# Kernel tuning notes

Hardware: AMD Instinct MI355X
Metric: run time of the kernel (lower is better)

## Reference

```python
import jax, jax.numpy as jnp
import numpy as np
import math

N, D_IN, D_OUT = 65536, 512, 512

def setup_inputs() -> dict:
    key = jax.random.key(0)
    k1, k2 = jax.random.split(key)
    x = jax.random.normal(k1, (N, D_IN), dtype=jnp.float32)
    stdv = 1.0 / math.sqrt(D_OUT)
    W = jax.random.uniform(k2, (D_OUT, D_IN), dtype=jnp.float32, minval=-stdv, maxval=stdv)
    W = W.at[:, 0].set(0.0)  # reset_parameters zeroes column 0 (step == in_features)
    b = jnp.zeros((D_OUT,), dtype=jnp.float32)
    scale = jnp.asarray(math.log(10.0), dtype=jnp.float32)  # learned log-scale param
    return {"x": x, "W": W, "b": b, "scale": scale}

def reference(x, W, b, scale):
    # Linear (dropout is identity at inference; nonlin is None)
    y = jnp.einsum('ni,oi->no', x, W) + b               # [N, D_OUT]
    time = jax.nn.sigmoid(y[..., :1]) * jnp.exp(scale) + 1.1   # [N, 1]
    x_narrow = y[..., 1:]                               # [N, D_OUT-1]
    denom = jnp.clip(jnp.sum(x_narrow * x_narrow, axis=-1, keepdims=True), 1e-8, None)
    s = (time * time - 1.0) / denom                     # [N, 1]
    return jnp.concatenate([time, x_narrow * jnp.sqrt(s)], axis=-1)
```

## Files before the change

### kernel.cpp

```cpp
#include <hip/hip_runtime.h>
#include <stdint.h>


typedef short short8 __attribute__((ext_vector_type(8)));
typedef unsigned short ushort4v __attribute__((ext_vector_type(4)));
typedef float f32x4 __attribute__((ext_vector_type(4)));

#define THREADS 512
#define BM 64
#define KTILES 16
#define LDS_W(buf) ((buf) * 32768)
#define LDS_X(buf) (65536 + (buf) * 4096)

__device__ __forceinline__ unsigned short f2bf(float f) {
  union { float f; uint32_t u; } v; v.f = f;
  uint32_t u = v.u;
  return (unsigned short)((u + 0x7FFFu + ((u >> 16) & 1u)) >> 16);
}

__device__ __forceinline__ void gload_lds16(const void* g, void* l) {
  __builtin_amdgcn_global_load_lds(
      (const __attribute__((address_space(1))) void*)g,
      (__attribute__((address_space(3))) void*)l, 16, 0, 0);
}

__global__ void wconv_kernel(const float* __restrict__ w,
                             unsigned short* __restrict__ wb) {
  const int i = (blockIdx.x * blockDim.x + threadIdx.x) * 4;
  float4 f = *(const float4*)(w + i);
  ushort4v h;
  h[0] = f2bf(f.x); h[1] = f2bf(f.y); h[2] = f2bf(f.z); h[3] = f2bf(f.w);
  *(ushort4v*)(wb + i) = h;
}

__global__ __launch_bounds__(THREADS, 4) void lorentz_kernel(
    const float* __restrict__ xg, const unsigned short* __restrict__ wb,
    const float* __restrict__ bg, const float* __restrict__ sg,
    float* __restrict__ out) {
  __shared__ __align__(16) char smem[73728];
  const int t = threadIdx.x;
  const int lane = t & 63;
  const int wid = t >> 6;
  const int wm = wid >> 2;
  const int wn = wid & 3;
  const int l15 = lane & 15;
  const int q = lane >> 4;
  const int bm = blockIdx.x * BM;
  const int swzl = ((l15 >> 1) & 3) << 4;

  const int wrow0 = t >> 2;
  const int wslog = (t & 3) ^ ((wrow0 >> 1) & 3);
  const unsigned short* wsrc0 = wb + wrow0 * 512 + wslog * 8;
  const int xm = t >> 3;
  const int xk4 = (t & 7) << 2;
  const float* xsrc0 = xg + (bm + xm) * 512 + xk4;
  const int xdst_off = xm * 64 + ((xk4 << 1) ^ ((((xm) >> 1) & 3) << 4));

  f32x4 acc[2][8];
  #pragma unroll
  for (int a = 0; a < 2; ++a)
    #pragma unroll
    for (int n = 0; n < 8; ++n)
      acc[a][n] = (f32x4){0.f, 0.f, 0.f, 0.f};

  auto stage = [&](int buf, int kt) {
    const float* xs = xsrc0 + kt * 32;
    float4 f0 = *(const float4*)xs;
    const unsigned short* ws = wsrc0 + kt * 32;
    char* wd = smem + LDS_W(buf) + t * 16;
    #pragma unroll
    for (int i = 0; i < 4; ++i)
      gload_lds16(ws + i * 65536, wd + i * 8192);
    ushort4v h;
    h[0] = f2bf(f0.x); h[1] = f2bf(f0.y); h[2] = f2bf(f0.z); h[3] = f2bf(f0.w);
    *(ushort4v*)(smem + LDS_X(buf) + xdst_off) = h;
  };

  auto compute = [&](int buf) {
    const char* wsrc = smem + LDS_W(buf);
    const char* xsrc = smem + LDS_X(buf);
    const int kb = q * 16;
    short8 af[2];
    #pragma unroll
    for (int mr = 0; mr < 2; ++mr) {
      const int row = wm * 32 + mr * 16 + l15;
      af[mr] = *(const short8*)(xsrc + row * 64 + (kb ^ swzl));
    }
    #pragma unroll
    for (int nr = 0; nr < 8; ++nr) {
      const int row = wn * 128 + nr * 16 + l15;
      const short8 bf = *(const short8*)(wsrc + row * 64 + (kb ^ swzl));
      acc[0][nr] = __builtin_amdgcn_mfma_f32_16x16x32_bf16(af[0], bf,
                                                           acc[0][nr], 0, 0, 0);
      acc[1][nr] = __builtin_amdgcn_mfma_f32_16x16x32_bf16(af[1], bf,
                                                           acc[1][nr], 0, 0, 0);
    }
  };

  stage(0, 0);
  __syncthreads();
  #pragma unroll
  for (int kt = 0; kt < KTILES; ++kt) {
    const int cur = kt & 1;
    if (kt + 1 < KTILES) stage(cur ^ 1, kt + 1);
    compute(cur);
    __syncthreads();
  }

  const float esc = __expf(sg[0]);
  float* red = (float*)smem;
  float* tsh = red + 64;
  if (t < 64) red[t] = 0.f;

  float bv[8];
  #pragma unroll
  for (int nr = 0; nr < 8; ++nr) bv[nr] = bg[wn * 128 + nr * 16 + l15];
  #pragma unroll
  for (int mr = 0; mr < 2; ++mr)
    #pragma unroll
    for (int nr = 0; nr < 8; ++nr)
      #pragma unroll
      for (int j = 0; j < 4; ++j)
        acc[mr][nr][j] += bv[nr];

  const bool col0 = (wn == 0) && (l15 == 0);
  float ps[2][4];
  #pragma unroll
  for (int mr = 0; mr < 2; ++mr)
    #pragma unroll
    for (int j = 0; j < 4; ++j) {
      float s = 0.f;
      #pragma unroll
      for (int nr = 0; nr < 8; ++nr) { const float v = acc[mr][nr][j]; s += v * v; }
      if (col0) { const float v = acc[mr][0][j]; s -= v * v; }
      ps[mr][j] = s;
    }
  #pragma unroll
  for (int msk = 1; msk < 16; msk <<= 1)
    #pragma unroll
    for (int mr = 0; mr < 2; ++mr)
      #pragma unroll
      for (int j = 0; j < 4; ++j)
        ps[mr][j] += __shfl_xor(ps[mr][j], msk, 64);

  __syncthreads();
  if (l15 == 0) {
    #pragma unroll
    for (int mr = 0; mr < 2; ++mr)
      #pragma unroll
      for (int j = 0; j < 4; ++j)
        atomicAdd(&red[wm * 32 + mr * 16 + q * 4 + j], ps[mr][j]);
  }
  if (col0) {
    #pragma unroll
    for (int mr = 0; mr < 2; ++mr)
      #pragma unroll
      for (int j = 0; j < 4; ++j) {
        const float y0 = acc[mr][0][j];
        const float sgm = 1.f / (1.f + __expf(-y0));
        tsh[wm * 32 + mr * 16 + q * 4 + j] = sgm * esc + 1.1f;
      }
  }
  __syncthreads();

  #pragma unroll
  for (int mr = 0; mr < 2; ++mr)
    #pragma unroll
    for (int j = 0; j < 4; ++j) {
      const int r = wm * 32 + mr * 16 + q * 4 + j;
      float denom = red[r];
      denom = denom < 1e-8f ? 1e-8f : denom;
      const float tt = tsh[r];
      const float coef = sqrtf((tt * tt - 1.f) / denom);
      float* orow = out + (size_t)(bm + r) * 512;
      #pragma unroll
      for (int nr = 0; nr < 8; ++nr) {
        const int c = wn * 128 + nr * 16 + l15;
        orow[c] = (c == 0) ? tt : acc[mr][nr][j] * coef;
      }
    }
}

extern "C" void kernel_launch(void* const* d_in, const int* in_sizes, int n_in,
                              void* d_out, int out_size, void* d_ws, size_t ws_size,
                              hipStream_t stream) {
  const float* x = (const float*)d_in[0];
  const float* W = (const float*)d_in[1];
  const float* b = (const float*)d_in[2];
  const float* sc = (const float*)d_in[3];
  float* outp = (float*)d_out;
  unsigned short* wb = (unsigned short*)d_ws;

  wconv_kernel<<<256, 256, 0, stream>>>(W, wb);
  lorentz_kernel<<<65536 / BM, THREADS, 0, stream>>>(x, wb, b, sc, outp);
}
```

Before: 259.4 us.

## Switch to 32x32x16 MFMA with triple-buffered K=16 pipeline and prefetch distance two

Replaces the 16x16x32 MFMA tiling with 32x32x16 bf16 MFMAs (four accumulators per wave) and shrinks the K tile to 16. Staging is now triple-buffered with a prefetch distance of two, uses explicit waitcnt and barrier, and raises MFMA priority with setprio. The aim is to cut LDS traffic per FLOP, lower LDS footprint for better occupancy, and overlap global loads with compute. The cost is twice as many barriers per K, and the unswizzled LDS layout may cause bank conflicts.

```diff
diff --git a/kernel.cpp b/kernel.cpp
--- a/kernel.cpp
+++ b/kernel.cpp
@@ -3,14 +3,14 @@
 
 
 typedef short short8 __attribute__((ext_vector_type(8)));
+typedef float f32x16 __attribute__((ext_vector_type(16)));
 typedef unsigned short ushort4v __attribute__((ext_vector_type(4)));
-typedef float f32x4 __attribute__((ext_vector_type(4)));
 
 #define THREADS 512
 #define BM 64
-#define KTILES 16
-#define LDS_W(buf) ((buf) * 32768)
-#define LDS_X(buf) (65536 + (buf) * 4096)
+#define WTILE 16384
+#define XTILE 2048
+#define PHASE (WTILE + XTILE)
 
 __device__ __forceinline__ unsigned short f2bf(float f) {
   union { float f; uint32_t u; } v; v.f = f;
@@ -37,148 +37,151 @@
     const float* __restrict__ xg, const unsigned short* __restrict__ wb,
     const float* __restrict__ bg, const float* __restrict__ sg,
     float* __restrict__ out) {
-  __shared__ __align__(16) char smem[73728];
+  __shared__ __align__(16) char smem[3 * PHASE];
   const int t = threadIdx.x;
   const int lane = t & 63;
   const int wid = t >> 6;
   const int wm = wid >> 2;
   const int wn = wid & 3;
-  const int l15 = lane & 15;
-  const int q = lane >> 4;
+  const int l31 = lane & 31;
+  const int h = lane >> 5;
   const int bm = blockIdx.x * BM;
-  const int swzl = ((l15 >> 1) & 3) << 4;
 
-  const int wrow0 = t >> 2;
-  const int wslog = (t & 3) ^ ((wrow0 >> 1) & 3);
-  const unsigned short* wsrc0 = wb + wrow0 * 512 + wslog * 8;
-  const int xm = t >> 3;
-  const int xk4 = (t & 7) << 2;
-  const float* xsrc0 = xg + (bm + xm) * 512 + xk4;
-  const int xdst_off = xm * 64 + ((xk4 << 1) ^ ((((xm) >> 1) & 3) << 4));
+  char* const P0 = smem;
+  char* const P1 = smem + PHASE;
+  char* const P2 = smem + 2 * PHASE;
 
-  f32x4 acc[2][8];
+  const unsigned short* wsrc0 = wb + (t >> 1) * 512 + (t & 1) * 8;
+  const float* xsrc0 = xg + (size_t)(bm + (t >> 3)) * 512 + (t & 7) * 2;
+  const int wdst = t * 16;
+  const int xdst = WTILE + (t >> 3) * 32 + (t & 7) * 4;
+  const int aoff = WTILE + wm * 1024 + l31 * 32 + h * 16;
+  const int boff = (wn * 128 + l31) * 32 + h * 16;
+
+  f32x16 acc[4];
   #pragma unroll
-  for (int a = 0; a < 2; ++a)
+  for (int n = 0; n < 4; ++n)
     #pragma unroll
-    for (int n = 0; n < 8; ++n)
-      acc[a][n] = (f32x4){0.f, 0.f, 0.f, 0.f};
+    for (int j = 0; j < 16; ++j) acc[n][j] = 0.f;
 
-  auto stage = [&](int buf, int kt) {
-    const float* xs = xsrc0 + kt * 32;
-    float4 f0 = *(const float4*)xs;
-    const unsigned short* ws = wsrc0 + kt * 32;
-    char* wd = smem + LDS_W(buf) + t * 16;
-    #pragma unroll
-    for (int i = 0; i < 4; ++i)
-      gload_lds16(ws + i * 65536, wd + i * 8192);
-    ushort4v h;
-    h[0] = f2bf(f0.x); h[1] = f2bf(f0.y); h[2] = f2bf(f0.z); h[3] = f2bf(f0.w);
-    *(ushort4v*)(smem + LDS_X(buf) + xdst_off) = h;
+  {
+    float2 xv0 = *(const float2*)(xsrc0);
+    gload_lds16(wsrc0, P0 + wdst);
+    gload_lds16(wsrc0 + 131072, P0 + 8192 + wdst);
+    unsigned int p0 = (unsigned int)f2bf(xv0.x) | ((unsigned int)f2bf(xv0.y) << 16);
+    *(unsigned int*)(P0 + xdst) = p0;
+    float2 xv1 = *(const float2*)(xsrc0 + 16);
+    gload_lds16(wsrc0 + 16, P1 + wdst);
+    gload_lds16(wsrc0 + 16 + 131072, P1 + 8192 + wdst);
+    unsigned int p1 = (unsigned int)f2bf(xv1.x) | ((unsigned int)f2bf(xv1.y) << 16);
+    *(unsigned int*)(P1 + xdst) = p1;
+    asm volatile("s_waitcnt vmcnt(0) lgkmcnt(0)" ::: "memory");
+    __builtin_amdgcn_s_barrier();
+  }
+
+  auto body = [&](int kt, char* cur, char* nxt, bool drain) {
+    short8 af  = *(const short8*)(cur + aoff);
+    short8 bf0 = *(const short8*)(cur + boff);
+    short8 bf1 = *(const short8*)(cur + boff + 1024);
+    short8 bf2 = *(const short8*)(cur + boff + 2048);
+    short8 bf3 = *(const short8*)(cur + boff + 3072);
+    float2 xv;
+    if (nxt) {
+      xv = *(const float2*)(xsrc0 + (kt + 2) * 16);
+      gload_lds16(wsrc0 + (kt + 2) * 16, nxt + wdst);
+      gload_lds16(wsrc0 + (kt + 2) * 16 + 131072, nxt + 8192 + wdst);
+    }
+    __builtin_amdgcn_s_setprio(1);
+    acc[0] = __builtin_amdgcn_mfma_f32_32x32x16_bf16(af, bf0, acc[0], 0, 0, 0);
+    acc[1] = __builtin_amdgcn_mfma_f32_32x32x16_bf16(af, bf1, acc[1], 0, 0, 0);
+    acc[2] = __builtin_amdgcn_mfma_f32_32x32x16_bf16(af, bf2, acc[2], 0, 0, 0);
+    acc[3] = __builtin_amdgcn_mfma_f32_32x32x16_bf16(af, bf3, acc[3], 0, 0, 0);
+    __builtin_amdgcn_s_setprio(0);
+    if (nxt) {
+      unsigned int p = (unsigned int)f2bf(xv.x) | ((unsigned int)f2bf(xv.y) << 16);
+      *(unsigned int*)(nxt + xdst) = p;
+    }
+    if (drain)
+      asm volatile("s_waitcnt vmcnt(0) lgkmcnt(0)" ::: "memory");
+    else
+      asm volatile("s_waitcnt lgkmcnt(0)" ::: "memory");
+    __builtin_amdgcn_s_barrier();
   };
 
-  auto compute = [&](int buf) {
-    const char* wsrc = smem + LDS_W(buf);
-    const char* xsrc = smem + LDS_X(buf);
-    const int kb = q * 16;
-    short8 af[2];
-    #pragma unroll
-    for (int mr = 0; mr < 2; ++mr) {
-      const int row = wm * 32 + mr * 16 + l15;
-      af[mr] = *(const short8*)(xsrc + row * 64 + (kb ^ swzl));
-    }
-    #pragma unroll
-    for (int nr = 0; nr < 8; ++nr) {
-      const int row = wn * 128 + nr * 16 + l15;
-      const short8 bf = *(const short8*)(wsrc + row * 64 + (kb ^ swzl));
-      acc[0][nr] = __builtin_amdgcn_mfma_f32_16x16x32_bf16(af[0], bf,
-                                                           acc[0][nr], 0, 0, 0);
-      acc[1][nr] = __builtin_amdgcn_mfma_f32_16x16x32_bf16(af[1], bf,
-                                                           acc[1][nr], 0, 0, 0);
-    }
-  };
-
-  stage(0, 0);
-  __syncthreads();
-  #pragma unroll
-  for (int kt = 0; kt < KTILES; ++kt) {
-    const int cur = kt & 1;
-    if (kt + 1 < KTILES) stage(cur ^ 1, kt + 1);
-    compute(cur);
-    __syncthreads();
+  for (int kt = 0; kt < 30; kt += 3) {
+    body(kt,     P0, P2, false);
+    body(kt + 1, P1, P0, false);
+    body(kt + 2, P2, P1, false);
   }
+  body(30, P0, nullptr, true);
+  body(31, P1, nullptr, false);
 
   const float esc = __expf(sg[0]);
+  float bv[4];
+  #pragma unroll
+  for (int nr = 0; nr < 4; ++nr) bv[nr] = bg[wn * 128 + nr * 32 + l31];
+  #pragma unroll
+  for (int nr = 0; nr < 4; ++nr)
+    #pragma unroll
+    for (int j = 0; j < 16; ++j)
+      acc[nr][j] += bv[nr];
+
+  const bool c0 = (wn == 0) && (l31 == 0);
+  float ss[16];
+  #pragma unroll
+  for (int j = 0; j < 16; ++j) {
+    float s = 0.f;
+    #pragma unroll
+    for (int nr = 0; nr < 4; ++nr) { const float v = acc[nr][j]; s += v * v; }
+    if (c0) { const float v = acc[0][j]; s -= v * v; }
+    ss[j] = s;
+  }
+  #pragma unroll
+  for (int m = 1; m < 32; m <<= 1)
+    #pragma unroll
+    for (int j = 0; j < 16; ++j)
+      ss[j] += __shfl_xor(ss[j], m, 64);
+
   float* red = (float*)smem;
-  float* tsh = red + 64;
+  float* tsh = (float*)(smem + 256);
   if (t < 64) red[t] = 0.f;
-
-  float bv[8];
-  #pragma unroll
-  for (int nr = 0; nr < 8; ++nr) bv[nr] = bg[wn * 128 + nr * 16 + l15];
-  #pragma unroll
-  for (int mr = 0; mr < 2; ++mr)
+  __syncthreads();
+  if (l31 == 0) {
     #pragma unroll
-    for (int nr = 0; nr < 8; ++nr)
-      #pragma unroll
-      for (int j = 0; j < 4; ++j)
-        acc[mr][nr][j] += bv[nr];
-
-  const bool col0 = (wn == 0) && (l15 == 0);
-  float ps[2][4];
-  #pragma unroll
-  for (int mr = 0; mr < 2; ++mr)
+    for (int j = 0; j < 16; ++j) {
+      const int r = wm * 32 + (j & 3) + 8 * (j >> 2) + 4 * h;
+      atomicAdd(&red[r], ss[j]);
+    }
+  }
+  if (c0) {
     #pragma unroll
-    for (int j = 0; j < 4; ++j) {
-      float s = 0.f;
-      #pragma unroll
-      for (int nr = 0; nr < 8; ++nr) { const float v = acc[mr][nr][j]; s += v * v; }
-      if (col0) { const float v = acc[mr][0][j]; s -= v * v; }
-      ps[mr][j] = s;
+    for (int j = 0; j < 16; ++j) {
+      const int r = wm * 32 + (j & 3) + 8 * (j >> 2) + 4 * h;
+      const float y0 = acc[0][j];
+      tsh[r] = esc / (1.f + __expf(-y0)) + 1.1f;
     }
-  #pragma unroll
-  for (int msk = 1; msk < 16; msk <<= 1)
-    #pragma unroll
-    for (int mr = 0; mr < 2; ++mr)
-      #pragma unroll
-      for (int j = 0; j < 4; ++j)
-        ps[mr][j] += __shfl_xor(ps[mr][j], msk, 64);
-
-  __syncthreads();
-  if (l15 == 0) {
-    #pragma unroll
-    for (int mr = 0; mr < 2; ++mr)
-      #pragma unroll
-      for (int j = 0; j < 4; ++j)
-        atomicAdd(&red[wm * 32 + mr * 16 + q * 4 + j], ps[mr][j]);
-  }
-  if (col0) {
-    #pragma unroll
-    for (int mr = 0; mr < 2; ++mr)
-      #pragma unroll
-      for (int j = 0; j < 4; ++j) {
-        const float y0 = acc[mr][0][j];
-        const float sgm = 1.f / (1.f + __expf(-y0));
-        tsh[wm * 32 + mr * 16 + q * 4 + j] = sgm * esc + 1.1f;
-      }
   }
   __syncthreads();
 
   #pragma unroll
-  for (int mr = 0; mr < 2; ++mr)
+  for (int g = 0; g < 4; ++g) {
+    const int rbase = wm * 32 + 8 * g + 4 * h;
+    const float4 r4 = *(const float4*)(red + rbase);
+    const float4 t4 = *(const float4*)(tsh + rbase);
     #pragma unroll
     for (int j = 0; j < 4; ++j) {
-      const int r = wm * 32 + mr * 16 + q * 4 + j;
-      float denom = red[r];
+      float denom = (&r4.x)[j];
       denom = denom < 1e-8f ? 1e-8f : denom;
-      const float tt = tsh[r];
+      const float tt = (&t4.x)[j];
       const float coef = sqrtf((tt * tt - 1.f) / denom);
-      float* orow = out + (size_t)(bm + r) * 512;
+      float* orow = out + (size_t)(bm + rbase + j) * 512;
       #pragma unroll
-      for (int nr = 0; nr < 8; ++nr) {
-        const int c = wn * 128 + nr * 16 + l15;
-        orow[c] = (c == 0) ? tt : acc[mr][nr][j] * coef;
+      for (int nr = 0; nr < 4; ++nr) {
+        const int c = wn * 128 + nr * 32 + l31;
+        orow[c] = (c == 0) ? tt : acc[nr][4 * g + j] * coef;
       }
     }
+  }
 }
 
 extern "C" void kernel_launch(void* const* d_in, const int* in_sizes, int n_in,
```

Measured after the change: 308.0 us. 18.7% more time.
